# Kernel tuning notes

Measured on AMD Instinct MI355X. Metric: run time of the kernel, lower is better.

## Reference

```python
import jax, jax.numpy as jnp
import numpy as np

INPUT_DIM = 128
OUTPUT_DIM = 256
BATCH = 4096

def setup_inputs() -> dict:
    key = jax.random.key(0)
    k_x, k_w1, k_b1, k_w2, k_b2 = jax.random.split(key, 5)
    d = INPUT_DIM
    h = 2 * OUTPUT_DIM
    x = jax.random.normal(k_x, (BATCH, d), dtype=jnp.float32)
    # Linear weights stored as [in, out]; scale ~ torch default init
    W1 = jax.random.uniform(k_w1, (d * d, h), dtype=jnp.float32, minval=-1, maxval=1) / np.sqrt(d * d)
    b1 = jax.random.uniform(k_b1, (h,), dtype=jnp.float32, minval=-1, maxval=1) / np.sqrt(d * d)
    W2 = jax.random.uniform(k_w2, (h, OUTPUT_DIM), dtype=jnp.float32, minval=-1, maxval=1) / np.sqrt(h)
    b2 = jax.random.uniform(k_b2, (OUTPUT_DIM,), dtype=jnp.float32, minval=-1, maxval=1) / np.sqrt(h)
    return {"x": x, "W1": W1, "b1": b1, "W2": W2, "b2": b2}

def reference(x, W1, b1, W2, b2):
    B, d = x.shape
    # torch bmm of the two expanded copies: tp[b,i,j] = sum_k x[b,i]*x[b,j] = d * x[b,i]*x[b,j]
    tp = jnp.asarray(d, x.dtype) * jnp.einsum('bi,bj->bij', x, x)  # [B, d, d]
    flat = tp.reshape(B, d * d)
    h = jax.nn.relu(flat @ W1 + b1)  # [B, 2*output_dim]
    return h @ W2 + b2               # [B, output_dim]
```

## Files before the change

### kernel.cpp

```cpp
#include <hip/hip_runtime.h>
#include <hip/hip_bf16.h>


typedef __attribute__((ext_vector_type(8))) short short8;
typedef __attribute__((ext_vector_type(4))) float floatx4;

__device__ __forceinline__ unsigned short f2bf(float f) {
    union { float f; unsigned int u; } v; v.f = f;
    unsigned int r = v.u + 0x7fffu + ((v.u >> 16) & 1u);
    return (unsigned short)(r >> 16);
}
__device__ __forceinline__ float bf2f(unsigned short b) {
    union { unsigned int u; float f; } v; v.u = ((unsigned int)b) << 16;
    return v.f;
}

__global__ __launch_bounds__(256) void prep_kernel(
    const float* __restrict__ W1, unsigned short* __restrict__ W1Tp,
    const float* __restrict__ W2, unsigned short* __restrict__ W2T) {
    __shared__ float tile[64][65];
    const int blk = blockIdx.x;
    const int tr = threadIdx.x >> 4;
    const int tc4 = (threadIdx.x & 15) * 4;
    if (blk < 2048) {
        const int k0 = (blk & 255) * 64;
        const int c0 = (blk >> 8) * 64;
#pragma unroll
        for (int p = 0; p < 4; ++p) {
            int k = p * 16 + tr;
            float4 v = *(const float4*)(W1 + (long)(k0 + k) * 512 + c0 + tc4);
            tile[k][tc4 + 0] = v.x; tile[k][tc4 + 1] = v.y;
            tile[k][tc4 + 2] = v.z; tile[k][tc4 + 3] = v.w;
        }
        __syncthreads();
        const int lane = threadIdx.x & 63;
        const int w = threadIdx.x >> 6;
        const int m = lane & 15, quad = lane >> 4;
#pragma unroll
        for (int pass = 0; pass < 2; ++pass) {
            int chunk = w * 2 + pass;
            int kcL = chunk & 1, c16L = chunk >> 1;
            union { unsigned short s[8]; uint4 u; } o;
#pragma unroll
            for (int j = 0; j < 8; ++j)
                o.s[j] = f2bf(tile[kcL * 32 + quad * 8 + j][c16L * 16 + m]);
            long c16g = (c0 >> 4) + c16L;
            long kcg  = (k0 >> 5) + kcL;
            *(uint4*)(W1Tp + (c16g * 512 + kcg) * 512 + lane * 8) = o.u;
        }
    } else {
        const int t = blk - 2048;
        const int r0 = (t & 7) * 64, c0 = (t >> 3) * 64;
        const int R = 512, C = 256;
#pragma unroll
        for (int p = 0; p < 4; ++p) {
            int r = p * 16 + tr;
            float4 v = *(const float4*)(W2 + (long)(r0 + r) * C + c0 + tc4);
            tile[r][tc4 + 0] = v.x; tile[r][tc4 + 1] = v.y;
            tile[r][tc4 + 2] = v.z; tile[r][tc4 + 3] = v.w;
        }
        __syncthreads();
#pragma unroll
        for (int p = 0; p < 4; ++p) {
            int c = p * 16 + tr;
            union { unsigned short s[4]; uint2 u; } pk;
#pragma unroll
            for (int e = 0; e < 4; ++e) pk.s[e] = f2bf(tile[tc4 + e][c]);
            *(uint2*)(W2T + (long)(c0 + c) * R + r0 + tc4) = pk.u;
        }
    }
}


#define A_STEP(Ac00, Ac01, Ac10, Ac11, I)                                  \
    {                                                                      \
        float xi[8];                                                       \
        _Pragma("unroll")                                                  \
        for (int tn = 0; tn < 8; ++tn)                                     \
            xi[tn] = xT[bLloc + tn * 16][(I)];                             \
        _Pragma("unroll")                                                  \
        for (int tn = 0; tn < 8; ++tn) {                                   \
            floatx4 t0 = __builtin_amdgcn_mfma_f32_16x16x32_bf16(          \
                Ac00, Xf[0][tn], zero4, 0, 0, 0);                          \
            t0 = __builtin_amdgcn_mfma_f32_16x16x32_bf16(                  \
                Ac01, Xf[1][tn], t0, 0, 0, 0);                             \
            acc[0][tn] += xi[tn] * t0;                                     \
            floatx4 t1 = __builtin_amdgcn_mfma_f32_16x16x32_bf16(          \
                Ac10, Xf[0][tn], zero4, 0, 0, 0);                          \
            t1 = __builtin_amdgcn_mfma_f32_16x16x32_bf16(                  \
                Ac11, Xf[1][tn], t1, 0, 0, 0);                             \
            acc[1][tn] += xi[tn] * t1;                                     \
        }                                                                  \
        const int p_ = ((I) + 4) & 31;  \
        Ac00 = *(const short8*)(aB00 + (long)p_ * 2048);                   \
        Ac01 = *(const short8*)(aB01 + (long)p_ * 2048);                   \
        Ac10 = *(const short8*)(aB10 + (long)p_ * 2048);                   \
        Ac11 = *(const short8*)(aB11 + (long)p_ * 2048);                   \
    }

__global__ __launch_bounds__(256, 2) void gemm1_kernel(
    const float* __restrict__ x,
    const unsigned short* __restrict__ W1Tp,
    unsigned short* __restrict__ Pb) {
    __shared__ float xT[256][34];
    const int tid = threadIdx.x;
    const int n = blockIdx.x;
    const int L = (n & 7) * 64 + (n >> 3);
    const int b0 = (L & 15) * 256;
    const int c0 = ((L >> 4) & 7) * 64;
    const int zi = L >> 7;
    const int i0 = zi * 32;

    for (int idx = tid; idx < 256 * 32; idx += 256) {
        int bL = idx >> 5, iL = idx & 31;
        xT[bL][iL] = x[(long)(b0 + bL) * 128 + i0 + iL];
    }
    __syncthreads();

    const int wid = tid >> 6;
    const int wm = wid >> 1, wn = wid & 1;
    const int lane = tid & 63;
    const int n16 = lane & 15, quad = lane >> 4;
    const int bBase = b0 + wn * 128;
    const int c16base = (c0 >> 4) + wm * 2;
    const int bLloc = wn * 128 + n16;

    floatx4 acc[2][8];
#pragma unroll
    for (int tm = 0; tm < 2; ++tm)
#pragma unroll
        for (int tn = 0; tn < 8; ++tn) acc[tm][tn] = (floatx4){0.f, 0.f, 0.f, 0.f};
    const floatx4 zero4 = (floatx4){0.f, 0.f, 0.f, 0.f};

#pragma unroll
    for (int jh = 0; jh < 2; ++jh) {
        short8 Xf[2][8];
#pragma unroll
        for (int ks = 0; ks < 2; ++ks)
#pragma unroll
            for (int tn = 0; tn < 8; ++tn) {
                const float* xp = x + (long)(bBase + tn * 16 + n16) * 128
                                    + jh * 64 + ks * 32 + quad * 8;
                float4 v0 = *(const float4*)xp;
                float4 v1 = *(const float4*)(xp + 4);
                short8 f;
                f[0] = (short)f2bf(v0.x); f[1] = (short)f2bf(v0.y);
                f[2] = (short)f2bf(v0.z); f[3] = (short)f2bf(v0.w);
                f[4] = (short)f2bf(v1.x); f[5] = (short)f2bf(v1.y);
                f[6] = (short)f2bf(v1.z); f[7] = (short)f2bf(v1.w);
                Xf[ks][tn] = f;
            }
        const unsigned short* aB00 = W1Tp
            + ((long)(c16base + 0) * 512 + (long)i0 * 4 + jh * 2 + 0) * 512
            + lane * 8;
        const unsigned short* aB01 = aB00 + 512;
        const unsigned short* aB10 = W1Tp
            + ((long)(c16base + 1) * 512 + (long)i0 * 4 + jh * 2 + 0) * 512
            + lane * 8;
        const unsigned short* aB11 = aB10 + 512;

        short8 A0_00 = *(const short8*)(aB00);
        short8 A0_01 = *(const short8*)(aB01);
        short8 A0_10 = *(const short8*)(aB10);
        short8 A0_11 = *(const short8*)(aB11);
        short8 A1_00 = *(const short8*)(aB00 + 1 * 2048);
        short8 A1_01 = *(const short8*)(aB01 + 1 * 2048);
        short8 A1_10 = *(const short8*)(aB10 + 1 * 2048);
        short8 A1_11 = *(const short8*)(aB11 + 1 * 2048);
        short8 A2_00 = *(const short8*)(aB00 + 2 * 2048);
        short8 A2_01 = *(const short8*)(aB01 + 2 * 2048);
        short8 A2_10 = *(const short8*)(aB10 + 2 * 2048);
        short8 A2_11 = *(const short8*)(aB11 + 2 * 2048);
        short8 A3_00 = *(const short8*)(aB00 + 3 * 2048);
        short8 A3_01 = *(const short8*)(aB01 + 3 * 2048);
        short8 A3_10 = *(const short8*)(aB10 + 3 * 2048);
        short8 A3_11 = *(const short8*)(aB11 + 3 * 2048);

#pragma unroll 1
        for (int ib = 0; ib < 8; ++ib) {
            const int i = ib * 4;
            A_STEP(A0_00, A0_01, A0_10, A0_11, i + 0)
            A_STEP(A1_00, A1_01, A1_10, A1_11, i + 1)
            A_STEP(A2_00, A2_01, A2_10, A2_11, i + 2)
            A_STEP(A3_00, A3_01, A3_10, A3_11, i + 3)
        }
    }

#pragma unroll
    for (int tm = 0; tm < 2; ++tm)
#pragma unroll
        for (int tn = 0; tn < 8; ++tn) {
            int ct = c16base + tm;
            int bt = (bBase >> 4) + tn;
            union { unsigned short s[4]; uint2 u; } pk;
#pragma unroll
            for (int r = 0; r < 4; ++r) pk.s[r] = f2bf(acc[tm][tn][r]);
            *(uint2*)(Pb + (((long)(zi * 32 + ct) * 256 + bt) * 64 + lane) * 4)
                = pk.u;
        }
}

__global__ __launch_bounds__(256) void tail_kernel(
    const unsigned short* __restrict__ Pb,
    const float* __restrict__ b1,
    const unsigned short* __restrict__ W2T,
    const float* __restrict__ b2,
    float* __restrict__ out) {
    __shared__ unsigned short hL[16][516];
    __shared__ float b1s[512];
    const int tid = threadIdx.x;
    const int bt = blockIdx.x;
    b1s[tid] = b1[tid];
    b1s[tid + 256] = b1[tid + 256];
    __syncthreads();

    const int w = tid >> 6, lane = tid & 63;
    const int n16 = lane & 15, quad = lane >> 4;

#pragma unroll
    for (int cc = 0; cc < 8; ++cc) {
        const int ct = cc * 4 + w;
        float s0 = 0.f, s1 = 0.f, s2 = 0.f, s3 = 0.f;
#pragma unroll
        for (int z = 0; z < 4; ++z) {
            uint2 u = *(const uint2*)(Pb
                + (((long)(z * 32 + ct) * 256 + bt) * 64 + lane) * 4);
            s0 += bf2f((unsigned short)(u.x & 0xffff));
            s1 += bf2f((unsigned short)(u.x >> 16));
            s2 += bf2f((unsigned short)(u.y & 0xffff));
            s3 += bf2f((unsigned short)(u.y >> 16));
        }
        const int c = ct * 16 + quad * 4;
        float v0 = fmaxf(fmaf(128.f, s0, b1s[c + 0]), 0.f);
        float v1 = fmaxf(fmaf(128.f, s1, b1s[c + 1]), 0.f);
        float v2 = fmaxf(fmaf(128.f, s2, b1s[c + 2]), 0.f);
        float v3 = fmaxf(fmaf(128.f, s3, b1s[c + 3]), 0.f);
        union { unsigned short s[4]; uint2 u; } pk;
        pk.s[0] = f2bf(v0); pk.s[1] = f2bf(v1);
        pk.s[2] = f2bf(v2); pk.s[3] = f2bf(v3);
        *(uint2*)&hL[n16][c] = pk.u;
    }
    __syncthreads();

    const int o0 = w * 64;
    floatx4 acc[4];
#pragma unroll
    for (int tn = 0; tn < 4; ++tn) acc[tn] = (floatx4){0.f, 0.f, 0.f, 0.f};

#pragma unroll 4
    for (int ks = 0; ks < 16; ++ks) {
        short8 Af, Bf[4];
        {
            const unsigned short* p = &hL[n16][ks * 32 + quad * 8];
            union { uint2 u[2]; short8 s; } cvt;
            cvt.u[0] = *(const uint2*)p;
            cvt.u[1] = *(const uint2*)(p + 4);
            Af = cvt.s;
        }
#pragma unroll
        for (int tn = 0; tn < 4; ++tn)
            Bf[tn] = *(const short8*)(W2T + (long)(o0 + tn * 16 + n16) * 512
                                      + ks * 32 + quad * 8);
#pragma unroll
        for (int tn = 0; tn < 4; ++tn)
            acc[tn] = __builtin_amdgcn_mfma_f32_16x16x32_bf16(
                Af, Bf[tn], acc[tn], 0, 0, 0);
    }
#pragma unroll
    for (int tn = 0; tn < 4; ++tn) {
        float bias = b2[o0 + tn * 16 + n16];
#pragma unroll
        for (int r = 0; r < 4; ++r)
            out[(long)(bt * 16 + quad * 4 + r) * 256
                + o0 + tn * 16 + n16] = acc[tn][r] + bias;
    }
}

extern "C" void kernel_launch(void* const* d_in, const int* in_sizes, int n_in,
                              void* d_out, int out_size, void* d_ws, size_t ws_size,
                              hipStream_t stream) {
    const float* x  = (const float*)d_in[0];
    const float* W1 = (const float*)d_in[1];
    const float* b1 = (const float*)d_in[2];
    const float* W2 = (const float*)d_in[3];
    const float* b2 = (const float*)d_in[4];
    float* out = (float*)d_out;

    char* ws = (char*)d_ws;
    unsigned short* W1Tp = (unsigned short*)(ws);
    unsigned short* W2T  = (unsigned short*)(ws + 16777216);
    unsigned short* Pb   = (unsigned short*)(ws + 16777216 + 262144);

    prep_kernel<<<dim3(2080), 256, 0, stream>>>(W1, W1Tp, W2, W2T);
    gemm1_kernel<<<dim3(512), 256, 0, stream>>>(x, W1Tp, Pb);
    tail_kernel<<<dim3(256), 256, 0, stream>>>(Pb, b1, W2T, b2, out);
}
```

Before: 170.3 us.

## Exploit symmetry of outer product to fold W1 and halve GEMM1 K

The outer product x⊗x is symmetric, so W1[i,j] and W1[j,i] are summed into one upper-triangular packed bf16 weight during prep. The main GEMM then runs only over i<=j pairs, split into off-diagonal and diagonal blocks balanced across four z-groups. This roughly halves the MFMA work and the W1 bytes streamed in GEMM1. Prep still reads all of W1 but writes a smaller packed buffer. The cost is complex indexing and an extra pass over the diagonal blocks.

```diff
diff --git a/kernel.cpp b/kernel.cpp
--- a/kernel.cpp
+++ b/kernel.cpp
@@ -16,63 +16,96 @@
 }
 
 __global__ __launch_bounds__(256) void prep_kernel(
-    const float* __restrict__ W1, unsigned short* __restrict__ W1Tp,
+    const float* __restrict__ W1, unsigned short* __restrict__ W1p,
     const float* __restrict__ W2, unsigned short* __restrict__ W2T) {
+    __shared__ float Asm[4][32][64];
+    __shared__ float Bsm[32][4][64];
     __shared__ float tile[64][65];
-    const int blk = blockIdx.x;
-    const int tr = threadIdx.x >> 4;
-    const int tc4 = (threadIdx.x & 15) * 4;
-    if (blk < 2048) {
-        const int k0 = (blk & 255) * 64;
-        const int c0 = (blk >> 8) * 64;
-#pragma unroll
-        for (int p = 0; p < 4; ++p) {
-            int k = p * 16 + tr;
-            float4 v = *(const float4*)(W1 + (long)(k0 + k) * 512 + c0 + tc4);
-            tile[k][tc4 + 0] = v.x; tile[k][tc4 + 1] = v.y;
-            tile[k][tc4 + 2] = v.z; tile[k][tc4 + 3] = v.w;
+    const int bx = blockIdx.x;
+    const int tid = threadIdx.x;
+    if (bx < 640) {
+        const int u = bx >> 6;
+        const int rem = bx & 63;
+        const int isub = rem >> 3, cb = rem & 7;
+        const int z  = (u < 4) ? 0 : (u < 7) ? 1 : (u < 9) ? 2 : 3;
+        const int kc = (u < 4) ? u : (u < 7) ? (u - 3) : (u < 9) ? (u - 5) : 3;
+        int base, stride;
+        if (z == 0)                 { base = (kc >> 1) * 64 + (kc & 1); stride = 2; }
+        else if (z == 1 && kc < 3)  { base = 128 + (kc - 1);            stride = 2; }
+        else if (z == 1)            { base = 256;                       stride = 1; }
+        else if (z == 2)            { base = 192 + (kc - 2);            stride = 2; }
+        else                        { base = 288;                       stride = 1; }
+        const int i0g = z * 32 + isub * 4;
+        const int j0g = kc * 32;
+        const int c0 = cb * 64;
+#pragma unroll
+        for (int it = 0; it < 8; ++it) {
+            int idx = tid + it * 256;
+            int r = idx >> 4;
+            int c4 = (idx & 15) * 4;
+            {   int iL = r >> 5, jL = r & 31;
+                float4 v = *(const float4*)(W1
+                    + ((long)(i0g + iL) * 128 + (j0g + jL)) * 512 + c0 + c4);
+                Asm[iL][jL][c4 + 0] = v.x; Asm[iL][jL][c4 + 1] = v.y;
+                Asm[iL][jL][c4 + 2] = v.z; Asm[iL][jL][c4 + 3] = v.w;
+            }
+            {   int jL = r >> 2, iL = r & 3;
+                float4 v = *(const float4*)(W1
+                    + ((long)(j0g + jL) * 128 + (i0g + iL)) * 512 + c0 + c4);
+                Bsm[jL][iL][c4 + 0] = v.x; Bsm[jL][iL][c4 + 1] = v.y;
+                Bsm[jL][iL][c4 + 2] = v.z; Bsm[jL][iL][c4 + 3] = v.w;
+            }
         }
         __syncthreads();
-        const int lane = threadIdx.x & 63;
-        const int w = threadIdx.x >> 6;
+        const int w = tid >> 6, lane = tid & 63;
         const int m = lane & 15, quad = lane >> 4;
-#pragma unroll
-        for (int pass = 0; pass < 2; ++pass) {
-            int chunk = w * 2 + pass;
-            int kcL = chunk & 1, c16L = chunk >> 1;
-            union { unsigned short s[8]; uint4 u; } o;
-#pragma unroll
-            for (int j = 0; j < 8; ++j)
-                o.s[j] = f2bf(tile[kcL * 32 + quad * 8 + j][c16L * 16 + m]);
-            long c16g = (c0 >> 4) + c16L;
-            long kcg  = (k0 >> 5) + kcL;
-            *(uint4*)(W1Tp + (c16g * 512 + kcg) * 512 + lane * 8) = o.u;
+        const int c16 = cb * 4 + w;
+        const int cl = w * 16 + m;
+#pragma unroll
+        for (int iL = 0; iL < 4; ++iL) {
+            const int ig = i0g + iL;
+            union { unsigned short s[8]; uint4 uu; } o;
+#pragma unroll
+            for (int e = 0; e < 8; ++e) {
+                int jL = quad * 8 + e;
+                int jg = j0g + jL;
+                float v;
+                if (jg > ig)      v = Asm[iL][jL][cl] + Bsm[jL][iL][cl];
+                else if (jg == ig) v = Asm[iL][jL][cl];
+                else               v = 0.f;
+                o.s[e] = f2bf(v);
+            }
+            const int il = isub * 4 + iL;
+            const long col = base + (long)il * stride;
+            *(uint4*)(W1p + ((long)c16 * 320 + col) * 512 + lane * 8) = o.uu;
         }
     } else {
-        const int t = blk - 2048;
+        const int t = bx - 640;
         const int r0 = (t & 7) * 64, c0 = (t >> 3) * 64;
         const int R = 512, C = 256;
-#pragma unroll
-        for (int p = 0; p < 4; ++p) {
-            int r = p * 16 + tr;
+        const int tr = tid >> 4;
+        const int tc4 = (tid & 15) * 4;
+#pragma unroll
+        for (int pp = 0; pp < 4; ++pp) {
+            int r = pp * 16 + tr;
             float4 v = *(const float4*)(W2 + (long)(r0 + r) * C + c0 + tc4);
             tile[r][tc4 + 0] = v.x; tile[r][tc4 + 1] = v.y;
             tile[r][tc4 + 2] = v.z; tile[r][tc4 + 3] = v.w;
         }
         __syncthreads();
 #pragma unroll
-        for (int p = 0; p < 4; ++p) {
-            int c = p * 16 + tr;
+        for (int pp = 0; pp < 4; ++pp) {
+            int cc = pp * 16 + tr;
             union { unsigned short s[4]; uint2 u; } pk;
 #pragma unroll
-            for (int e = 0; e < 4; ++e) pk.s[e] = f2bf(tile[tc4 + e][c]);
-            *(uint2*)(W2T + (long)(c0 + c) * R + r0 + tc4) = pk.u;
-        }
-    }
-}
-
-
-#define A_STEP(Ac00, Ac01, Ac10, Ac11, I)                                  \
+            for (int e = 0; e < 4; ++e) pk.s[e] = f2bf(tile[tc4 + e][cc]);
+            *(uint2*)(W2T + (long)(c0 + cc) * R + r0 + tc4) = pk.u;
+        }
+    }
+}
+
+
+#define A_STEP2(Ac00, Ac01, Ac10, Ac11, I)                                 \
     {                                                                      \
         float xi[8];                                                       \
         _Pragma("unroll")                                                  \
@@ -92,28 +125,56 @@
             acc[1][tn] += xi[tn] * t1;                                     \
         }                                                                  \
         const int p_ = ((I) + 4) & 31;  \
-        Ac00 = *(const short8*)(aB00 + (long)p_ * 2048);                   \
-        Ac01 = *(const short8*)(aB01 + (long)p_ * 2048);                   \
-        Ac10 = *(const short8*)(aB10 + (long)p_ * 2048);                   \
-        Ac11 = *(const short8*)(aB11 + (long)p_ * 2048);                   \
-    }
-
-__global__ __launch_bounds__(256, 2) void gemm1_kernel(
+        Ac00 = *(const short8*)(aB00 + (long)p_ * 1024);                   \
+        Ac01 = *(const short8*)(aB01 + (long)p_ * 1024);                   \
+        Ac10 = *(const short8*)(aB10 + (long)p_ * 1024);                   \
+        Ac11 = *(const short8*)(aB11 + (long)p_ * 1024);                   \
+    }
+
+#define H_STEP(Ac0, Ac1, I)                                                \
+    {                                                                      \
+        float xi[8];                                                       \
+        _Pragma("unroll")                                                  \
+        for (int tn = 0; tn < 8; ++tn)                                     \
+            xi[tn] = xT[bLloc + tn * 16][(I)];                             \
+        _Pragma("unroll")                                                  \
+        for (int tn = 0; tn < 8; ++tn) {                                   \
+            floatx4 t0 = __builtin_amdgcn_mfma_f32_16x16x32_bf16(          \
+                Ac0, Xf[0][tn], zero4, 0, 0, 0);                           \
+            acc[0][tn] += xi[tn] * t0;                                     \
+            floatx4 t1 = __builtin_amdgcn_mfma_f32_16x16x32_bf16(          \
+                Ac1, Xf[0][tn], zero4, 0, 0, 0);                           \
+            acc[1][tn] += xi[tn] * t1;                                     \
+        }                                                                  \
+        const int p_ = ((I) + 4) & 15;                                     \
+        Ac0 = *(const short8*)(aC0 + (long)p_ * 512);                      \
+        Ac1 = *(const short8*)(aC1 + (long)p_ * 512);                      \
+    }
+
+__global__ __launch_bounds__(256, 2) void gemm_sym_kernel(
     const float* __restrict__ x,
-    const unsigned short* __restrict__ W1Tp,
+    const unsigned short* __restrict__ W1p,
     unsigned short* __restrict__ Pb) {
     __shared__ float xT[256][34];
     const int tid = threadIdx.x;
     const int n = blockIdx.x;
     const int L = (n & 7) * 64 + (n >> 3);
-    const int b0 = (L & 15) * 256;
-    const int c0 = ((L >> 4) & 7) * 64;
-    const int zi = L >> 7;
-    const int i0 = zi * 32;
+    const int bx = L & 15;
+    const int s = L >> 4;
+    const int g = s & 3;
+    const int cb = s >> 2;
+    const int b0 = bx * 256;
+    const int c0 = cb * 64;
+    const int i0_2 = (g < 2) ? 0 : (g - 1) * 32;
+    const int i0_1 = 32 + (g & 1) * 16 + (g >> 1) * 64;
+    const int col2 = g * 64;
+    const int col1 = 256 + g * 16;
+    const int jc0 = (g == 0) ? 0 : (g == 2) ? 1 : 2;
+    const int jc1 = (g == 0) ? 1 : (g == 2) ? 2 : 3;
 
     for (int idx = tid; idx < 256 * 32; idx += 256) {
         int bL = idx >> 5, iL = idx & 31;
-        xT[bL][iL] = x[(long)(b0 + bL) * 128 + i0 + iL];
+        xT[bL][iL] = x[(long)(b0 + bL) * 128 + i0_2 + iL];
     }
     __syncthreads();
 
@@ -132,57 +193,101 @@
         for (int tn = 0; tn < 8; ++tn) acc[tm][tn] = (floatx4){0.f, 0.f, 0.f, 0.f};
     const floatx4 zero4 = (floatx4){0.f, 0.f, 0.f, 0.f};
 
-#pragma unroll
-    for (int jh = 0; jh < 2; ++jh) {
-        short8 Xf[2][8];
-#pragma unroll
-        for (int ks = 0; ks < 2; ++ks)
-#pragma unroll
-            for (int tn = 0; tn < 8; ++tn) {
-                const float* xp = x + (long)(bBase + tn * 16 + n16) * 128
-                                    + jh * 64 + ks * 32 + quad * 8;
-                float4 v0 = *(const float4*)xp;
-                float4 v1 = *(const float4*)(xp + 4);
-                short8 f;
-                f[0] = (short)f2bf(v0.x); f[1] = (short)f2bf(v0.y);
-                f[2] = (short)f2bf(v0.z); f[3] = (short)f2bf(v0.w);
-                f[4] = (short)f2bf(v1.x); f[5] = (short)f2bf(v1.y);
-                f[6] = (short)f2bf(v1.z); f[7] = (short)f2bf(v1.w);
-                Xf[ks][tn] = f;
-            }
-        const unsigned short* aB00 = W1Tp
-            + ((long)(c16base + 0) * 512 + (long)i0 * 4 + jh * 2 + 0) * 512
-            + lane * 8;
+    short8 Xf[2][8];
+#pragma unroll
+    for (int ks = 0; ks < 2; ++ks) {
+        const int jc = ks ? jc1 : jc0;
+#pragma unroll
+        for (int tn = 0; tn < 8; ++tn) {
+            const float* xp = x + (long)(bBase + tn * 16 + n16) * 128
+                                + jc * 32 + quad * 8;
+            float4 v0 = *(const float4*)xp;
+            float4 v1 = *(const float4*)(xp + 4);
+            short8 f;
+            f[0] = (short)f2bf(v0.x); f[1] = (short)f2bf(v0.y);
+            f[2] = (short)f2bf(v0.z); f[3] = (short)f2bf(v0.w);
+            f[4] = (short)f2bf(v1.x); f[5] = (short)f2bf(v1.y);
+            f[6] = (short)f2bf(v1.z); f[7] = (short)f2bf(v1.w);
+            Xf[ks][tn] = f;
+        }
+    }
+
+    {
+        const unsigned short* aB00 = W1p
+            + ((long)(c16base + 0) * 320 + col2) * 512 + lane * 8;
         const unsigned short* aB01 = aB00 + 512;
-        const unsigned short* aB10 = W1Tp
-            + ((long)(c16base + 1) * 512 + (long)i0 * 4 + jh * 2 + 0) * 512
-            + lane * 8;
+        const unsigned short* aB10 = W1p
+            + ((long)(c16base + 1) * 320 + col2) * 512 + lane * 8;
         const unsigned short* aB11 = aB10 + 512;
 
         short8 A0_00 = *(const short8*)(aB00);
         short8 A0_01 = *(const short8*)(aB01);
         short8 A0_10 = *(const short8*)(aB10);
         short8 A0_11 = *(const short8*)(aB11);
-        short8 A1_00 = *(const short8*)(aB00 + 1 * 2048);
-        short8 A1_01 = *(const short8*)(aB01 + 1 * 2048);
-        short8 A1_10 = *(const short8*)(aB10 + 1 * 2048);
-        short8 A1_11 = *(const short8*)(aB11 + 1 * 2048);
-        short8 A2_00 = *(const short8*)(aB00 + 2 * 2048);
-        short8 A2_01 = *(const short8*)(aB01 + 2 * 2048);
-        short8 A2_10 = *(const short8*)(aB10 + 2 * 2048);
-        short8 A2_11 = *(const short8*)(aB11 + 2 * 2048);
-        short8 A3_00 = *(const short8*)(aB00 + 3 * 2048);
-        short8 A3_01 = *(const short8*)(aB01 + 3 * 2048);
-        short8 A3_10 = *(const short8*)(aB10 + 3 * 2048);
-        short8 A3_11 = *(const short8*)(aB11 + 3 * 2048);
+        short8 A1_00 = *(const short8*)(aB00 + 1 * 1024);
+        short8 A1_01 = *(const short8*)(aB01 + 1 * 1024);
+        short8 A1_10 = *(const short8*)(aB10 + 1 * 1024);
+        short8 A1_11 = *(const short8*)(aB11 + 1 * 1024);
+        short8 A2_00 = *(const short8*)(aB00 + 2 * 1024);
+        short8 A2_01 = *(const short8*)(aB01 + 2 * 1024);
+        short8 A2_10 = *(const short8*)(aB10 + 2 * 1024);
+        short8 A2_11 = *(const short8*)(aB11 + 2 * 1024);
+        short8 A3_00 = *(const short8*)(aB00 + 3 * 1024);
+        short8 A3_01 = *(const short8*)(aB01 + 3 * 1024);
+        short8 A3_10 = *(const short8*)(aB10 + 3 * 1024);
+        short8 A3_11 = *(const short8*)(aB11 + 3 * 1024);
 
 #pragma unroll 1
         for (int ib = 0; ib < 8; ++ib) {
             const int i = ib * 4;
-            A_STEP(A0_00, A0_01, A0_10, A0_11, i + 0)
-            A_STEP(A1_00, A1_01, A1_10, A1_11, i + 1)
-            A_STEP(A2_00, A2_01, A2_10, A2_11, i + 2)
-            A_STEP(A3_00, A3_01, A3_10, A3_11, i + 3)
+            A_STEP2(A0_00, A0_01, A0_10, A0_11, i + 0)
+            A_STEP2(A1_00, A1_01, A1_10, A1_11, i + 1)
+            A_STEP2(A2_00, A2_01, A2_10, A2_11, i + 2)
+            A_STEP2(A3_00, A3_01, A3_10, A3_11, i + 3)
+        }
+    }
+
+    __syncthreads();
+    for (int idx = tid; idx < 256 * 16; idx += 256) {
+        int bL = idx >> 4, iL = idx & 15;
+        xT[bL][iL] = x[(long)(b0 + bL) * 128 + i0_1 + iL];
+    }
+    __syncthreads();
+#pragma unroll
+    for (int tn = 0; tn < 8; ++tn) {
+        const float* xp = x + (long)(bBase + tn * 16 + n16) * 128
+                            + 3 * 32 + quad * 8;
+        float4 v0 = *(const float4*)xp;
+        float4 v1 = *(const float4*)(xp + 4);
+        short8 f;
+        f[0] = (short)f2bf(v0.x); f[1] = (short)f2bf(v0.y);
+        f[2] = (short)f2bf(v0.z); f[3] = (short)f2bf(v0.w);
+        f[4] = (short)f2bf(v1.x); f[5] = (short)f2bf(v1.y);
+        f[6] = (short)f2bf(v1.z); f[7] = (short)f2bf(v1.w);
+        Xf[0][tn] = f;
+    }
+
+    {
+        const unsigned short* aC0 = W1p
+            + ((long)(c16base + 0) * 320 + col1) * 512 + lane * 8;
+        const unsigned short* aC1 = W1p
+            + ((long)(c16base + 1) * 320 + col1) * 512 + lane * 8;
+        short8 C0_0 = *(const short8*)(aC0);
+        short8 C0_1 = *(const short8*)(aC1);
+        short8 C1_0 = *(const short8*)(aC0 + 1 * 512);
+        short8 C1_1 = *(const short8*)(aC1 + 1 * 512);
+        short8 C2_0 = *(const short8*)(aC0 + 2 * 512);
+        short8 C2_1 = *(const short8*)(aC1 + 2 * 512);
+        short8 C3_0 = *(const short8*)(aC0 + 3 * 512);
+        short8 C3_1 = *(const short8*)(aC1 + 3 * 512);
+
+#pragma unroll 1
+        for (int ib = 0; ib < 4; ++ib) {
+            const int i = ib * 4;
+            H_STEP(C0_0, C0_1, i + 0)
+            H_STEP(C1_0, C1_1, i + 1)
+            H_STEP(C2_0, C2_1, i + 2)
+            H_STEP(C3_0, C3_1, i + 3)
         }
     }
 
@@ -195,7 +300,7 @@
             union { unsigned short s[4]; uint2 u; } pk;
 #pragma unroll
             for (int r = 0; r < 4; ++r) pk.s[r] = f2bf(acc[tm][tn][r]);
-            *(uint2*)(Pb + (((long)(zi * 32 + ct) * 256 + bt) * 64 + lane) * 4)
+            *(uint2*)(Pb + (((long)(g * 32 + ct) * 256 + bt) * 64 + lane) * 4)
                 = pk.u;
         }
 }
@@ -287,11 +392,11 @@
     float* out = (float*)d_out;
 
     char* ws = (char*)d_ws;
-    unsigned short* W1Tp = (unsigned short*)(ws);
-    unsigned short* W2T  = (unsigned short*)(ws + 16777216);
-    unsigned short* Pb   = (unsigned short*)(ws + 16777216 + 262144);
-
-    prep_kernel<<<dim3(2080), 256, 0, stream>>>(W1, W1Tp, W2, W2T);
-    gemm1_kernel<<<dim3(512), 256, 0, stream>>>(x, W1Tp, Pb);
+    unsigned short* W1p = (unsigned short*)(ws);
+    unsigned short* W2T = (unsigned short*)(ws + 10485760);
+    unsigned short* Pb  = (unsigned short*)(ws + 10485760 + 262144);
+
+    prep_kernel<<<dim3(672), 256, 0, stream>>>(W1, W1p, W2, W2T);
+    gemm_sym_kernel<<<dim3(512), 256, 0, stream>>>(x, W1p, Pb);
     tail_kernel<<<dim3(256), 256, 0, stream>>>(Pb, b1, W2T, b2, out);
 }
```

Result: faster. 155.0 us (-9.0%).
